# Performance work log

Hardware: AMD Instinct MI355X
Metric: run time of the kernel (lower is better)

## Reference

```python
import jax, jax.numpy as jnp
import numpy as np

DIM = 1024
NUM_HEADS = 16
HEAD_DIM = DIM // NUM_HEADS


def setup_inputs() -> dict:
    key = jax.random.key(0)
    k1, k2, k3, k4, k5 = jax.random.split(key, 5)
    x = jax.random.normal(k1, (4, 4096, DIM), dtype=jnp.float32)
    # truncnormal002 init ~ std 0.02; plain normal*0.02 is a faithful stand-in for testing
    w_qkv = jax.random.normal(k2, (3 * DIM, DIM), dtype=jnp.float32) * 0.02
    b_qkv = jnp.zeros((3 * DIM,), dtype=jnp.float32)
    w_proj = jax.random.normal(k3, (DIM, DIM), dtype=jnp.float32) * 0.02
    b_proj = jnp.zeros((DIM,), dtype=jnp.float32)
    return {"x": x, "w_qkv": w_qkv, "b_qkv": b_qkv, "w_proj": w_proj, "b_proj": b_proj}


def reference(x, w_qkv, b_qkv, w_proj, b_proj):
    bs, seqlen, dim = x.shape
    # qkv projection (torch Linear: x @ W^T + b)
    qkv = x @ w_qkv.T + b_qkv  # [bs, seqlen, 3*dim]
    qkv = qkv.reshape(bs, seqlen, 3, NUM_HEADS, HEAD_DIM)
    qkv = jnp.transpose(qkv, (2, 0, 3, 1, 4))  # [3, bs, heads, seqlen, head_dim]
    q, k, v = qkv[0], qkv[1], qkv[2]
    q = jax.nn.softmax(q, axis=-1) * (HEAD_DIM ** -0.5)  # softmax over head_dim
    k = jax.nn.softmax(k, axis=-2)                        # softmax over seqlen
    # linear attention: kv state is [heads, head_dim, head_dim]
    kv = jnp.einsum('bhsd,bhse->bhde', k, v)  # k^T @ v
    out = jnp.einsum('bhsd,bhde->bhse', q, kv)  # q @ kv
    out = jnp.transpose(out, (0, 2, 1, 3)).reshape(bs, seqlen, dim)
    return out @ w_proj.T + b_proj
```

## Files before the change

### kernel.cpp

```cpp
#include <hip/hip_runtime.h>
#include <hip/hip_bf16.h>
#include <stdint.h>


#define DIM 1024
#define NH 16
#define HD 64
#define BSZ 4
#define SEQ 4096
#define MTOT (BSZ*SEQ)
#define NQKV (3*DIM)
#define QSCALE 0.125f
#define LOG2E 1.4426950408889634f

typedef __attribute__((ext_vector_type(8))) short bf16x8;
typedef __attribute__((ext_vector_type(4))) float f32x4;
typedef __attribute__((ext_vector_type(4))) float float4_t;
typedef __attribute__((ext_vector_type(4))) unsigned short ushort4_t;
typedef __attribute__((ext_vector_type(8))) unsigned short ushort8_t;

__device__ __forceinline__ unsigned short f2bf(float f) {
  uint32_t u = __builtin_bit_cast(uint32_t, f);
  u += 0x7fffu + ((u >> 16) & 1u);
  return (unsigned short)(u >> 16);
}
__device__ __forceinline__ float bf2f(unsigned short h) {
  uint32_t u = ((uint32_t)h) << 16;
  return __builtin_bit_cast(float, u);
}

#define GLD16(gp, lp) __builtin_amdgcn_global_load_lds( \
    (const __attribute__((address_space(1))) void*)(gp), \
    (__attribute__((address_space(3))) void*)(lp), 16, 0, 0)

__global__ __launch_bounds__(256) void cvt_kernel(
    const float* __restrict__ in, unsigned short* __restrict__ out, long n) {
  long i = ((long)blockIdx.x * 256 + threadIdx.x) * 8;
  if (i >= n) return;
  float4_t a = *(const float4_t*)(in + i);
  float4_t b = *(const float4_t*)(in + i + 4);
  ushort8_t r;
  r[0] = f2bf(a[0]); r[1] = f2bf(a[1]); r[2] = f2bf(a[2]); r[3] = f2bf(a[3]);
  r[4] = f2bf(b[0]); r[5] = f2bf(b[1]); r[6] = f2bf(b[2]); r[7] = f2bf(b[3]);
  *(ushort8_t*)(out + i) = r;
}

__global__ __launch_bounds__(256) void zero_f32(float* __restrict__ p) {
  int i = (blockIdx.x * 256 + threadIdx.x) * 4;
  *(float4_t*)(p + i) = (float4_t){0.f, 0.f, 0.f, 0.f};
}

#define BM 128
#define BN 128
#define BK 32

template <int MODE>
__global__ __launch_bounds__(256, 2)
void gemm_bt(const unsigned short* __restrict__ Aall,
             const unsigned short* __restrict__ Ball,
             const float* __restrict__ bias,
             unsigned short* __restrict__ Oq,
             unsigned short* __restrict__ Okt,
             unsigned short* __restrict__ Ovt,
             float* __restrict__ Of,
             int M, int Kdim)
{
  __shared__ __align__(16) unsigned short As[BM * BK];
  __shared__ __align__(16) unsigned short Bs[BN * BK];

  const int t = threadIdx.x;
  const int lane = t & 63;
  const int wid = t >> 6;
  const int wr = wid >> 1, wc = wid & 1;

  const int m0 = blockIdx.x * BM;
  const int n0 = blockIdx.y * BN;

  const unsigned short* A = Aall;
  const unsigned short* B = Ball;
  if (MODE == 1) {
    A += (size_t)blockIdx.z * M * Kdim;
    B += (size_t)blockIdx.z * DIM * Kdim;
  }

  const int r0 = t >> 2;
  const int r1 = r0 + 64;
  const int sseg = ((t & 3) ^ (r0 & 3)) * 8;
  const unsigned short* gA0 = A + (size_t)(m0 + r0) * Kdim + sseg;
  const unsigned short* gA1 = A + (size_t)(m0 + r1) * Kdim + sseg;
  const unsigned short* gB0 = B + (size_t)(n0 + r0) * Kdim + sseg;
  const unsigned short* gB1 = B + (size_t)(n0 + r1) * Kdim + sseg;

  char* lA0 = (char*)As + wid * 1024;
  char* lA1 = (char*)As + 4096 + wid * 1024;
  char* lB0 = (char*)Bs + wid * 1024;
  char* lB1 = (char*)Bs + 4096 + wid * 1024;

  const int arow = wr * 64 + (lane & 15);
  const int brow = wc * 64 + (lane & 15);
  const int aoff = ((lane >> 4) ^ (lane & 3)) * 8;

  f32x4 acc[4][4];
#pragma unroll
  for (int i = 0; i < 4; ++i)
#pragma unroll
    for (int j = 0; j < 4; ++j) acc[i][j] = (f32x4){0.f, 0.f, 0.f, 0.f};

  const int KT = Kdim / BK;
  for (int kt = 0; kt < KT; ++kt) {
    GLD16(gA0, lA0); GLD16(gA1, lA1);
    GLD16(gB0, lB0); GLD16(gB1, lB1);
    gA0 += BK; gA1 += BK; gB0 += BK; gB1 += BK;
    __syncthreads();
    bf16x8 af[4], bfr[4];
#pragma unroll
    for (int i = 0; i < 4; ++i)
      af[i] = *(const bf16x8*)(As + (arow + i * 16) * BK + aoff);
#pragma unroll
    for (int j = 0; j < 4; ++j)
      bfr[j] = *(const bf16x8*)(Bs + (brow + j * 16) * BK + aoff);
#pragma unroll
    for (int i = 0; i < 4; ++i)
#pragma unroll
      for (int j = 0; j < 4; ++j)
        acc[i][j] = __builtin_amdgcn_mfma_f32_16x16x32_bf16(af[i], bfr[j], acc[i][j], 0, 0, 0);
    __syncthreads();
  }

#pragma unroll
  for (int i = 0; i < 4; ++i) {
    const int rowb = m0 + wr * 64 + i * 16 + (lane >> 4) * 4;
#pragma unroll
    for (int j = 0; j < 4; ++j) {
      const int col = n0 + wc * 64 + j * 16 + (lane & 15);
      const float bv = bias[col];
#pragma unroll
      for (int r = 0; r < 4; ++r) {
        const float val = acc[i][j][r] + bv;
        const int rr = rowb + r;
        if (MODE == 0) {
          const unsigned short obf = f2bf(val);
          const int b = rr >> 12, s = rr & 4095;
          if (col < DIM) {
            Oq[(size_t)rr * DIM + col] = obf;
          } else if (col < 2 * DIM) {
            const int n2 = col - DIM;
            const size_t bhd = (size_t)(b * NH + (n2 >> 6)) * HD + (n2 & 63);
            Okt[bhd * SEQ + s] = obf;
          } else {
            const int n2 = col - 2 * DIM;
            const size_t bhd = (size_t)(b * NH + (n2 >> 6)) * HD + (n2 & 63);
            Ovt[bhd * SEQ + s] = obf;
          }
        } else {
          Of[(size_t)blockIdx.z * M * DIM + (size_t)rr * DIM + col] = val;
        }
      }
    }
  }
}

__global__ __launch_bounds__(256)
void colstats_rows(const unsigned short* __restrict__ Kt,
                   float* __restrict__ mcol, float* __restrict__ zcol)
{
  const int row = blockIdx.x * 4 + (threadIdx.x >> 6);
  const int lane = threadIdx.x & 63;
  const unsigned short* p = Kt + (size_t)row * SEQ + lane * 8;
  bf16x8 v[8];
#pragma unroll
  for (int c = 0; c < 8; ++c) v[c] = *(const bf16x8*)(p + c * 512);
  float mx = -1e30f;
#pragma unroll
  for (int c = 0; c < 8; ++c)
#pragma unroll
    for (int j = 0; j < 8; ++j) mx = fmaxf(mx, bf2f((unsigned short)v[c][j]));
#pragma unroll
  for (int off = 1; off < 64; off <<= 1) mx = fmaxf(mx, __shfl_xor(mx, off, 64));
  float s = 0.f;
#pragma unroll
  for (int c = 0; c < 8; ++c)
#pragma unroll
    for (int j = 0; j < 8; ++j) s += __expf(bf2f((unsigned short)v[c][j]) - mx);
#pragma unroll
  for (int off = 1; off < 64; off <<= 1) s += __shfl_xor(s, off, 64);
  if (lane == 0) { mcol[row] = mx; zcol[row] = s; }
}

__global__ __launch_bounds__(256)
void kv_mfma(const unsigned short* __restrict__ Kt, const unsigned short* __restrict__ Vt,
             const float* __restrict__ mcol, float* __restrict__ kvws)
{
  __shared__ __align__(16) unsigned short Ks[64 * 128];
  __shared__ __align__(16) unsigned short Vs[64 * 128];
  const int bh = blockIdx.x, ch = blockIdx.y;
  const int t = threadIdx.x, lane = t & 63, w = t >> 6;
  const int r = lane & 15, g = lane >> 4;

  const float mc = mcol[bh * 64 + 16 * w + r] * LOG2E;
  const size_t kbase = (size_t)bh * 64 * SEQ;

  f32x4 acc[4];
#pragma unroll
  for (int j = 0; j < 4; ++j) acc[j] = (f32x4){0.f, 0.f, 0.f, 0.f};

  int s0 = ch * 512;
  for (int st = 0; st < 4; ++st, s0 += 128) {
#pragma unroll
    for (int q = 0; q < 4; ++q) {
      const int d = 16 * w + 4 * q + g;
      const int gl = r ^ (d & 7);
      const size_t go = kbase + (size_t)d * SEQ + s0 + gl * 8;
      GLD16(Kt + go, Ks + (16 * w + 4 * q) * 128);
      GLD16(Vt + go, Vs + (16 * w + 4 * q) * 128);
    }
    __syncthreads();
#pragma unroll
    for (int ks = 0; ks < 4; ++ks) {
      const int coff = (((4 * ks + g) ^ (r & 7)) * 8);
      bf16x8 a = *(const bf16x8*)(Ks + (16 * w + r) * 128 + coff);
      bf16x8 ae;
#pragma unroll
      for (int j = 0; j < 8; ++j) {
        float f = bf2f((unsigned short)a[j]);
        float p = exp2f(f * LOG2E - mc);
        ae[j] = (short)f2bf(p);
      }
#pragma unroll
      for (int jt = 0; jt < 4; ++jt) {
        bf16x8 b = *(const bf16x8*)(Vs + (16 * jt + r) * 128 + coff);
        acc[jt] = __builtin_amdgcn_mfma_f32_16x16x32_bf16(ae, b, acc[jt], 0, 0, 0);
      }
    }
    __syncthreads();
  }
#pragma unroll
  for (int jt = 0; jt < 4; ++jt)
#pragma unroll
    for (int reg = 0; reg < 4; ++reg)
      atomicAdd(&kvws[((size_t)bh * 64 + 16 * w + g * 4 + reg) * 64 + 16 * jt + r],
                acc[jt][reg]);
}

__global__ __launch_bounds__(256)
void mbt_kernel(const float* __restrict__ kvws, const float* __restrict__ zcol,
                const float* __restrict__ wproj, unsigned short* __restrict__ MbT)
{
  __shared__ float kvl[64][65];
  const int b = blockIdx.x, h = blockIdx.y, nb = blockIdx.z;
  const int t = threadIdx.x;
  const int bh = b * NH + h;
  for (int u = t; u < 4096; u += 256) {
    int d = u >> 6, e = u & 63;
    float inv = QSCALE / zcol[bh * 64 + d];
    kvl[d][e] = kvws[((size_t)bh * 64 + d) * 64 + e] * inv;
  }
  __syncthreads();
  const int n = nb * 64 + (t >> 2);
  const int dg = (t & 3) * 16;
  const float* wrow = wproj + (size_t)n * DIM + h * HD;
  float out[16];
#pragma unroll
  for (int i = 0; i < 16; ++i) out[i] = 0.f;
  for (int e = 0; e < 64; e += 4) {
    float4_t w4 = *(const float4_t*)(wrow + e);
#pragma unroll
    for (int i = 0; i < 16; ++i)
      out[i] += w4[0] * kvl[dg + i][e] + w4[1] * kvl[dg + i][e + 1]
              + w4[2] * kvl[dg + i][e + 2] + w4[3] * kvl[dg + i][e + 3];
  }
  unsigned short* o = MbT + ((size_t)b * DIM + n) * DIM + h * HD + dg;
  ushort8_t o0, o1;
#pragma unroll
  for (int i = 0; i < 8; ++i) { o0[i] = f2bf(out[i]); o1[i] = f2bf(out[i + 8]); }
  *(ushort8_t*)(o) = o0;
  *(ushort8_t*)(o + 8) = o1;
}

__global__ __launch_bounds__(256)
void softmax_q(unsigned short* __restrict__ Q)
{
  const int t = threadIdx.x;
  const int lane = t & 63, wid = t >> 6;
  const size_t base = (((size_t)blockIdx.x * 4 + wid) * 256) + (size_t)lane * 4;
  ushort4_t q4 = *(const ushort4_t*)(Q + base);
  float x0 = bf2f(q4[0]), x1 = bf2f(q4[1]), x2 = bf2f(q4[2]), x3 = bf2f(q4[3]);
  float mx = fmaxf(fmaxf(x0, x1), fmaxf(x2, x3));
  for (int off = 1; off < 16; off <<= 1) mx = fmaxf(mx, __shfl_xor(mx, off, 16));
  float e0 = __expf(x0 - mx), e1 = __expf(x1 - mx);
  float e2 = __expf(x2 - mx), e3 = __expf(x3 - mx);
  float s = e0 + e1 + e2 + e3;
  for (int off = 1; off < 16; off <<= 1) s += __shfl_xor(s, off, 16);
  const float inv = 1.f / s;
  ushort4_t rr;
  rr[0] = f2bf(e0 * inv); rr[1] = f2bf(e1 * inv);
  rr[2] = f2bf(e2 * inv); rr[3] = f2bf(e3 * inv);
  *(ushort4_t*)(Q + base) = rr;
}

extern "C" void kernel_launch(void* const* d_in, const int* in_sizes, int n_in,
                              void* d_out, int out_size, void* d_ws, size_t ws_size,
                              hipStream_t stream)
{
  const float* x      = (const float*)d_in[0];
  const float* w_qkv  = (const float*)d_in[1];
  const float* b_qkv  = (const float*)d_in[2];
  const float* w_proj = (const float*)d_in[3];
  const float* b_proj = (const float*)d_in[4];
  float* out = (float*)d_out;

  char* ws = (char*)d_ws;
  size_t off = 0;
  auto alloc = [&](size_t bytes) -> void* {
    void* p = ws + off;
    off += (bytes + 255) & ~(size_t)255;
    return p;
  };
  unsigned short* xb   = (unsigned short*)alloc(2ull * MTOT * DIM);
  unsigned short* wqb  = (unsigned short*)alloc(2ull * NQKV * DIM);
  unsigned short* Qb   = (unsigned short*)alloc(2ull * MTOT * DIM);
  unsigned short* Ktb  = (unsigned short*)alloc(2ull * MTOT * DIM);
  unsigned short* Vtb  = (unsigned short*)alloc(2ull * MTOT * DIM);
  float* mcol  = (float*)alloc(4ull * 4096);
  float* zcol  = (float*)alloc(4ull * 4096);
  float* kvws  = (float*)alloc(4ull * 64 * 64 * 64);
  unsigned short* MbT = (unsigned short*)alloc(2ull * BSZ * DIM * DIM);
  if (off > ws_size) return;

  cvt_kernel<<<8192, 256, 0, stream>>>(x, xb, (long)MTOT * DIM);
  cvt_kernel<<<1536, 256, 0, stream>>>(w_qkv, wqb, (long)NQKV * DIM);

  gemm_bt<0><<<dim3(128, 24), 256, 0, stream>>>(xb, wqb, b_qkv, Qb, Ktb, Vtb,
                                                nullptr, MTOT, DIM);

  colstats_rows<<<1024, 256, 0, stream>>>(Ktb, mcol, zcol);

  zero_f32<<<256, 256, 0, stream>>>(kvws);
  kv_mfma<<<dim3(64, 8), 256, 0, stream>>>(Ktb, Vtb, mcol, kvws);
  mbt_kernel<<<dim3(4, 16, 16), 256, 0, stream>>>(kvws, zcol, w_proj, MbT);

  softmax_q<<<16384, 256, 0, stream>>>(Qb);

  gemm_bt<1><<<dim3(32, 8, 4), 256, 0, stream>>>(Qb, MbT, b_proj,
                                                 nullptr, nullptr, nullptr, out,
                                                 SEQ, DIM);
}
```

Baseline: 408.6 us.

## Replace GEMM with 256x256 double-buffered 8-wave pipelined MFMA kernel

Both GEMMs switch from a 128x128, BK=32, single-buffered kernel to a 512-thread 256x256-tile kernel with BK=64. It double-buffers in 128KB of LDS, interleaves global-to-LDS staging with MFMA phases, and uses explicit barriers, waitcnt and setprio. The QKV GEMM also gets a grid swizzle for L2 locality. The aim is more data reuse per tile and hiding global load latency behind matrix math. The trade-offs are heavy LDS use that limits occupancy to one block per CU, and some redundant wraparound prefetches at the end of the K loop.

```diff
diff --git a/kernel.cpp b/kernel.cpp
--- a/kernel.cpp
+++ b/kernel.cpp
@@ -50,31 +50,79 @@
   *(float4_t*)(p + i) = (float4_t){0.f, 0.f, 0.f, 0.f};
 }
 
-#define BM 128
-#define BN 128
-#define BK 32
+
+#define LDA_(TB, MREP, KS) (*(const bf16x8*)(lds + (TB)*65536 + \
+    (32*(MREP) + 16*wm + r4)*128 + ((((KS)*4 + g) ^ (r4 & 7))*16)))
+#define LDB_(TB, NREP, KS) (*(const bf16x8*)(lds + (TB)*65536 + 32768 + \
+    (wn*64 + (NREP)*16 + r4)*128 + ((((KS)*4 + g) ^ (r4 & 7))*16)))
+
+#define STAGE(SB, ISB, H, KT_) do { \
+    const unsigned short* _src = (ISB) ? B : A; \
+    const int _rb = ((ISB) ? n0 : m0) + (H) * 128; \
+    const unsigned short* _g0 = _src + (size_t)(_rb + srow) * Kdim + (KT_) * 64 + scol; \
+    const unsigned short* _g1 = _src + (size_t)(_rb + 64 + srow) * Kdim + (KT_) * 64 + scol; \
+    char* _l0 = lds + (SB) * 65536 + (ISB) * 32768 + (H) * 16384 + soff; \
+    GLD16(_g0, _l0); \
+    GLD16(_g1, _l0 + 8192); \
+  } while (0)
+
+#define MFMA_ __builtin_amdgcn_mfma_f32_16x16x32_bf16
+
+#define PHASE(TB, P, LOADB, SB, SISB, SH, SKT, GATE) do { \
+    if (LOADB) { \
+      b00 = LDB_(TB,0,0); b01 = LDB_(TB,0,1); b10 = LDB_(TB,1,0); b11 = LDB_(TB,1,1); \
+      b20 = LDB_(TB,2,0); b21 = LDB_(TB,2,1); b30 = LDB_(TB,3,0); b31 = LDB_(TB,3,1); \
+    } \
+    bf16x8 a00 = LDA_(TB,2*(P),0),   a01 = LDA_(TB,2*(P),1); \
+    bf16x8 a10 = LDA_(TB,2*(P)+1,0), a11 = LDA_(TB,2*(P)+1,1); \
+    STAGE(SB, SISB, SH, SKT); \
+    __builtin_amdgcn_sched_barrier(0); \
+    __builtin_amdgcn_s_barrier(); \
+    asm volatile("s_waitcnt lgkmcnt(0)" ::: "memory"); \
+    __builtin_amdgcn_sched_barrier(0); \
+    __builtin_amdgcn_s_setprio(1); \
+    acc[2*(P)][0]   = MFMA_(a00,b00,acc[2*(P)][0],0,0,0);   acc[2*(P)][0]   = MFMA_(a01,b01,acc[2*(P)][0],0,0,0); \
+    acc[2*(P)][1]   = MFMA_(a00,b10,acc[2*(P)][1],0,0,0);   acc[2*(P)][1]   = MFMA_(a01,b11,acc[2*(P)][1],0,0,0); \
+    acc[2*(P)][2]   = MFMA_(a00,b20,acc[2*(P)][2],0,0,0);   acc[2*(P)][2]   = MFMA_(a01,b21,acc[2*(P)][2],0,0,0); \
+    acc[2*(P)][3]   = MFMA_(a00,b30,acc[2*(P)][3],0,0,0);   acc[2*(P)][3]   = MFMA_(a01,b31,acc[2*(P)][3],0,0,0); \
+    acc[2*(P)+1][0] = MFMA_(a10,b00,acc[2*(P)+1][0],0,0,0); acc[2*(P)+1][0] = MFMA_(a11,b01,acc[2*(P)+1][0],0,0,0); \
+    acc[2*(P)+1][1] = MFMA_(a10,b10,acc[2*(P)+1][1],0,0,0); acc[2*(P)+1][1] = MFMA_(a11,b11,acc[2*(P)+1][1],0,0,0); \
+    acc[2*(P)+1][2] = MFMA_(a10,b20,acc[2*(P)+1][2],0,0,0); acc[2*(P)+1][2] = MFMA_(a11,b21,acc[2*(P)+1][2],0,0,0); \
+    acc[2*(P)+1][3] = MFMA_(a10,b30,acc[2*(P)+1][3],0,0,0); acc[2*(P)+1][3] = MFMA_(a11,b31,acc[2*(P)+1][3],0,0,0); \
+    __builtin_amdgcn_s_setprio(0); \
+    __builtin_amdgcn_sched_barrier(0); \
+    if (GATE) { asm volatile("s_waitcnt vmcnt(6)" ::: "memory"); } \
+    __builtin_amdgcn_s_barrier(); \
+    __builtin_amdgcn_sched_barrier(0); \
+  } while (0)
 
 template <int MODE>
-__global__ __launch_bounds__(256, 2)
-void gemm_bt(const unsigned short* __restrict__ Aall,
-             const unsigned short* __restrict__ Ball,
-             const float* __restrict__ bias,
-             unsigned short* __restrict__ Oq,
-             unsigned short* __restrict__ Okt,
-             unsigned short* __restrict__ Ovt,
-             float* __restrict__ Of,
-             int M, int Kdim)
-{
-  __shared__ __align__(16) unsigned short As[BM * BK];
-  __shared__ __align__(16) unsigned short Bs[BN * BK];
-
-  const int t = threadIdx.x;
-  const int lane = t & 63;
-  const int wid = t >> 6;
-  const int wr = wid >> 1, wc = wid & 1;
-
-  const int m0 = blockIdx.x * BM;
-  const int n0 = blockIdx.y * BN;
+__global__ __launch_bounds__(512, 2)
+void gemm8p(const unsigned short* __restrict__ Aall,
+            const unsigned short* __restrict__ Ball,
+            const float* __restrict__ bias,
+            unsigned short* __restrict__ Oq,
+            unsigned short* __restrict__ Okt,
+            unsigned short* __restrict__ Ovt,
+            float* __restrict__ Of,
+            int M, int Kdim)
+{
+  __shared__ __align__(16) char lds[131072];
+  const int t = threadIdx.x, l = t & 63, wid = t >> 6;
+  const int wm = wid >> 2, wn = wid & 3;
+  const int r4 = l & 15, g = l >> 4;
+
+  int bx, by;
+  if (MODE == 0) {
+    const int bid = blockIdx.y * gridDim.x + blockIdx.x;
+    const int cpx = (gridDim.x * gridDim.y) >> 3;
+    const int swz = (bid & 7) * cpx + (bid >> 3);
+    bx = swz % gridDim.x;
+    by = swz / gridDim.x;
+  } else {
+    bx = blockIdx.x; by = blockIdx.y;
+  }
+  const int m0 = bx * 256, n0 = by * 256;
 
   const unsigned short* A = Aall;
   const unsigned short* B = Ball;
@@ -83,78 +131,79 @@
     B += (size_t)blockIdx.z * DIM * Kdim;
   }
 
-  const int r0 = t >> 2;
-  const int r1 = r0 + 64;
-  const int sseg = ((t & 3) ^ (r0 & 3)) * 8;
-  const unsigned short* gA0 = A + (size_t)(m0 + r0) * Kdim + sseg;
-  const unsigned short* gA1 = A + (size_t)(m0 + r1) * Kdim + sseg;
-  const unsigned short* gB0 = B + (size_t)(n0 + r0) * Kdim + sseg;
-  const unsigned short* gB1 = B + (size_t)(n0 + r1) * Kdim + sseg;
-
-  char* lA0 = (char*)As + wid * 1024;
-  char* lA1 = (char*)As + 4096 + wid * 1024;
-  char* lB0 = (char*)Bs + wid * 1024;
-  char* lB1 = (char*)Bs + 4096 + wid * 1024;
-
-  const int arow = wr * 64 + (lane & 15);
-  const int brow = wc * 64 + (lane & 15);
-  const int aoff = ((lane >> 4) ^ (lane & 3)) * 8;
-
-  f32x4 acc[4][4];
-#pragma unroll
-  for (int i = 0; i < 4; ++i)
+  const int srow = wid * 8 + (l >> 3);
+  const int scol = ((l & 7) ^ (l >> 3)) * 8;
+  const int soff = wid * 1024;
+
+  f32x4 acc[8][4];
+#pragma unroll
+  for (int i = 0; i < 8; ++i)
 #pragma unroll
     for (int j = 0; j < 4; ++j) acc[i][j] = (f32x4){0.f, 0.f, 0.f, 0.f};
-
-  const int KT = Kdim / BK;
-  for (int kt = 0; kt < KT; ++kt) {
-    GLD16(gA0, lA0); GLD16(gA1, lA1);
-    GLD16(gB0, lB0); GLD16(gB1, lB1);
-    gA0 += BK; gA1 += BK; gB0 += BK; gB1 += BK;
-    __syncthreads();
-    bf16x8 af[4], bfr[4];
-#pragma unroll
-    for (int i = 0; i < 4; ++i)
-      af[i] = *(const bf16x8*)(As + (arow + i * 16) * BK + aoff);
-#pragma unroll
-    for (int j = 0; j < 4; ++j)
-      bfr[j] = *(const bf16x8*)(Bs + (brow + j * 16) * BK + aoff);
-#pragma unroll
-    for (int i = 0; i < 4; ++i)
-#pragma unroll
-      for (int j = 0; j < 4; ++j)
-        acc[i][j] = __builtin_amdgcn_mfma_f32_16x16x32_bf16(af[i], bfr[j], acc[i][j], 0, 0, 0);
-    __syncthreads();
-  }
-
-#pragma unroll
-  for (int i = 0; i < 4; ++i) {
-    const int rowb = m0 + wr * 64 + i * 16 + (lane >> 4) * 4;
-#pragma unroll
-    for (int j = 0; j < 4; ++j) {
-      const int col = n0 + wc * 64 + j * 16 + (lane & 15);
-      const float bv = bias[col];
-#pragma unroll
-      for (int r = 0; r < 4; ++r) {
-        const float val = acc[i][j][r] + bv;
-        const int rr = rowb + r;
-        if (MODE == 0) {
+  bf16x8 b00, b01, b10, b11, b20, b21, b30, b31;
+
+  STAGE(0, 1, 0, 0); STAGE(0, 1, 1, 0); STAGE(0, 0, 0, 0); STAGE(0, 0, 1, 0);
+  STAGE(1, 1, 0, 1); STAGE(1, 1, 1, 1); STAGE(1, 0, 0, 1);
+  asm volatile("s_waitcnt vmcnt(6)" ::: "memory");
+  __builtin_amdgcn_sched_barrier(0);
+  __builtin_amdgcn_s_barrier();
+  __builtin_amdgcn_sched_barrier(0);
+
+  const int KT = Kdim >> 6;
+  for (int it = 0; it < (KT >> 1); ++it) {
+    const int t1 = 2 * it + 1;
+    int t2 = 2 * it + 2; if (t2 >= KT) t2 -= KT;
+    int t3 = 2 * it + 3; if (t3 >= KT) t3 -= KT;
+    PHASE(0, 0, 1, 1, 0, 1, t1, 0);
+    PHASE(0, 1, 0, 0, 1, 0, t2, 0);
+    PHASE(0, 2, 0, 0, 1, 1, t2, 0);
+    PHASE(0, 3, 0, 0, 0, 0, t2, 1);
+    PHASE(1, 0, 1, 0, 0, 1, t2, 0);
+    PHASE(1, 1, 0, 1, 1, 0, t3, 0);
+    PHASE(1, 2, 0, 1, 1, 1, t3, 0);
+    PHASE(1, 3, 0, 1, 0, 0, t3, 1);
+  }
+
+  if (MODE == 0) {
+    const int region = n0 >> 10;
+    float bv[4];
+#pragma unroll
+    for (int j = 0; j < 4; ++j) bv[j] = bias[n0 + wn * 64 + j * 16 + r4];
+#pragma unroll
+    for (int mi = 0; mi < 8; ++mi) {
+      const int rowb = m0 + 32 * mi + 16 * wm + g * 4;
+#pragma unroll
+      for (int j = 0; j < 4; ++j) {
+        const int col = n0 + wn * 64 + j * 16 + r4;
+#pragma unroll
+        for (int r = 0; r < 4; ++r) {
+          const float val = acc[mi][j][r] + bv[j];
+          const int rr = rowb + r;
           const unsigned short obf = f2bf(val);
-          const int b = rr >> 12, s = rr & 4095;
-          if (col < DIM) {
+          if (region == 0) {
             Oq[(size_t)rr * DIM + col] = obf;
-          } else if (col < 2 * DIM) {
-            const int n2 = col - DIM;
+          } else {
+            const int n2 = col - region * DIM;
+            const int b = rr >> 12, s = rr & 4095;
             const size_t bhd = (size_t)(b * NH + (n2 >> 6)) * HD + (n2 & 63);
-            Okt[bhd * SEQ + s] = obf;
-          } else {
-            const int n2 = col - 2 * DIM;
-            const size_t bhd = (size_t)(b * NH + (n2 >> 6)) * HD + (n2 & 63);
-            Ovt[bhd * SEQ + s] = obf;
+            if (region == 1) Okt[bhd * SEQ + s] = obf;
+            else             Ovt[bhd * SEQ + s] = obf;
           }
-        } else {
-          Of[(size_t)blockIdx.z * M * DIM + (size_t)rr * DIM + col] = val;
         }
+      }
+    }
+  } else {
+    float* Ob = Of + (size_t)blockIdx.z * M * DIM;
+#pragma unroll
+    for (int mi = 0; mi < 8; ++mi) {
+      const int rowb = m0 + 32 * mi + 16 * wm + g * 4;
+#pragma unroll
+      for (int j = 0; j < 4; ++j) {
+        const int col = n0 + wn * 64 + j * 16 + r4;
+        const float bvj = bias[col];
+#pragma unroll
+        for (int r = 0; r < 4; ++r)
+          Ob[(size_t)(rowb + r) * DIM + col] = acc[mi][j][r] + bvj;
       }
     }
   }
@@ -330,8 +379,8 @@
   cvt_kernel<<<8192, 256, 0, stream>>>(x, xb, (long)MTOT * DIM);
   cvt_kernel<<<1536, 256, 0, stream>>>(w_qkv, wqb, (long)NQKV * DIM);
 
-  gemm_bt<0><<<dim3(128, 24), 256, 0, stream>>>(xb, wqb, b_qkv, Qb, Ktb, Vtb,
-                                                nullptr, MTOT, DIM);
+  gemm8p<0><<<dim3(64, 12), 512, 0, stream>>>(xb, wqb, b_qkv, Qb, Ktb, Vtb,
+                                              nullptr, MTOT, DIM);
 
   colstats_rows<<<1024, 256, 0, stream>>>(Ktb, mcol, zcol);
 
@@ -341,7 +390,7 @@
 
   softmax_q<<<16384, 256, 0, stream>>>(Qb);
 
-  gemm_bt<1><<<dim3(32, 8, 4), 256, 0, stream>>>(Qb, MbT, b_proj,
-                                                 nullptr, nullptr, nullptr, out,
-                                                 SEQ, DIM);
-}
+  gemm8p<1><<<dim3(16, 4, 4), 512, 0, stream>>>(Qb, MbT, b_proj,
+                                                nullptr, nullptr, nullptr, out,
+                                                SEQ, DIM);
+}
```

Result: no change. 403.4 us (-1.3%).
